# Optimization experiments

Measured on AMD Instinct MI355X. Metric: run time of the kernel, lower is better.

The kernel has to match this reference:

```python
import jax, jax.numpy as jnp
import numpy as np

B, N, OBS = 512, 64, 256
H1, H2 = 4, 4
D = 128            # embed/key dim (d_k_1 = d_k_2 = 128)
O1 = D // H1       # 32, per-head value dim stage 1
O2 = D // H2       # 32, per-head value dim stage 2
IN2 = O1 * H1      # 128, input dim to stage 2
FOUT = 16          # final_output_dim


def setup_inputs() -> dict:
    key = jax.random.key(0)
    ks = jax.random.split(key, 22)
    g = lambda k, shp: (jax.random.normal(k, shp, dtype=jnp.float32) * 0.05)
    inp = {
        "states": jax.random.normal(ks[0], (B, N, OBS), dtype=jnp.float32),
        # stage 1 per-head params, stacked over heads
        "E1_w": g(ks[1], (H1, D, OBS)), "E1_b": g(ks[2], (H1, D)),
        "K1_w": g(ks[3], (H1, D, D)),   "K1_b": g(ks[4], (H1, D)),
        "Q1_w": g(ks[5], (H1, D, D)),   "Q1_b": g(ks[6], (H1, D)),
        "V1_w": g(ks[7], (H1, O1, D)),  "V1_b": g(ks[8], (H1, O1)),
        # stage 2 per-head params
        "E2_w": g(ks[9], (H2, D, IN2)), "E2_b": g(ks[10], (H2, D)),
        "K2_w": g(ks[11], (H2, D, D)),  "K2_b": g(ks[12], (H2, D)),
        "Q2_w": g(ks[13], (H2, D, D)),  "Q2_b": g(ks[14], (H2, D)),
        "V2_w": g(ks[15], (H2, O2, D)), "V2_b": g(ks[16], (H2, O2)),
        # final MLP policy head
        "F1_w": g(ks[17], (64, O2 * H2)), "F1_b": g(ks[18], (64,)),
        "F2_w": g(ks[19], (FOUT, 64)),    "F2_b": g(ks[20], (FOUT,)),
    }
    return inp


def _attn_block(x, Ew, Eb, Kw, Kb, Qw, Qb, Vw, Vb, d_k):
    # x: [B,N,I]; all head loops batched via leading head axis h
    se = jax.nn.leaky_relu(jnp.einsum('bni,hdi->hbnd', x, Ew) + Eb[:, None, None, :])  # [h,B,N,D]
    k = jnp.einsum('hbnd,hed->hbne', se, Kw) + Kb[:, None, None, :]
    q = jnp.einsum('hbnd,hed->hbne', se, Qw) + Qb[:, None, None, :]
    w = jax.nn.softmax(jnp.einsum('hbne,hbme->hbnm', q, k) / jnp.sqrt(jnp.float32(d_k)), axis=-1)  # [h,B,N,N]
    v = jax.nn.leaky_relu(jnp.einsum('hbnd,hod->hbno', se, Vw) + Vb[:, None, None, :])  # [h,B,N,O]
    att = jnp.einsum('hbnm,hbmo->hbno', w, v)
    h, b, n, o = att.shape
    return jnp.transpose(att, (1, 2, 0, 3)).reshape(b, n, h * o), w


def reference(states, E1_w, E1_b, K1_w, K1_b, Q1_w, Q1_b, V1_w, V1_b,
              E2_w, E2_b, K2_w, K2_b, Q2_w, Q2_b, V2_w, V2_b,
              F1_w, F1_b, F2_w, F2_b):
    x1, w1 = _attn_block(states, E1_w, E1_b, K1_w, K1_b, Q1_w, Q1_b, V1_w, V1_b, D)
    x2, w2 = _attn_block(x1, E2_w, E2_b, K2_w, K2_b, Q2_w, Q2_b, V2_w, V2_b, D)
    h = jax.nn.leaky_relu(jnp.einsum('bnf,of->bno', x2, F1_w) + F1_b)
    policy = jax.nn.softmax(jnp.einsum('bno,po->bnp', h, F2_w) + F2_b, axis=-1)
    return policy, w1, w2
```

## Files before the change

kernel.cpp:

```cpp
#include <hip/hip_runtime.h>

typedef __attribute__((ext_vector_type(8))) short short8;
typedef __attribute__((ext_vector_type(4))) short short4v;
typedef __attribute__((ext_vector_type(4))) float f32x4;

#define MFMA(a, b, c) __builtin_amdgcn_mfma_f32_16x16x32_bf16((a), (b), (c), 0, 0, 0)

__device__ __forceinline__ short f2bf(float f) {
    union { float f; unsigned u; } v; v.f = f;
    unsigned r = v.u + 0x7fffu + ((v.u >> 16) & 1u);
    return (short)(r >> 16);
}
__device__ __forceinline__ float bf2f(short s) {
    union { unsigned u; float f; } v; v.u = ((unsigned)(unsigned short)s) << 16; return v.f;
}

struct ConvArgs { const float* src[10]; int end[10]; };

__global__ __launch_bounds__(256) void convert_weights_kernel(ConvArgs a, short* __restrict__ dst) {
    int i4 = blockIdx.x * 256 + threadIdx.x;
    int seg = 0;
#pragma unroll
    for (int s = 0; s < 9; s++) seg += (i4 >= a.end[s]) ? 1 : 0;
    int base = (seg == 0) ? 0 : a.end[seg - 1];
    float4 v = ((const float4*)a.src[seg])[i4 - base];
    short4v o; o.x = f2bf(v.x); o.y = f2bf(v.y); o.z = f2bf(v.z); o.w = f2bf(v.w);
    *(short4v*)(dst + (size_t)i4 * 4) = o;
}

#define KQ_LD  136
#define VT_LD  72
#define W_LD   72
#define OFF_K  0
#define OFF_Q  8704
#define OFF_SE 17408
#define OFF_VT 26112
#define OFF_W  8704
#define SMEM_SHORTS 28416

template<int IN, bool XF32>
__global__ __launch_bounds__(256) void attn_stage_kernel(
    const void* __restrict__ xin,
    const short* __restrict__ Ew, const float* __restrict__ Eb,
    const short* __restrict__ Kw, const float* __restrict__ Kb,
    const short* __restrict__ Qw, const float* __restrict__ Qb,
    const short* __restrict__ Vw, const float* __restrict__ Vb,
    float* __restrict__ w_out,
    short* __restrict__ x_out)
{
    __shared__ short sm[SMEM_SHORTS];
    const int tid  = threadIdx.x;
    const int b    = blockIdx.x >> 2;
    const int h    = blockIdx.x & 3;
    const int wv   = tid >> 6;
    const int lane = tid & 63;
    const int quad = lane >> 4;
    const int l16  = lane & 15;
    const int XLD  = IN + 8;

    if constexpr (XF32) {
        const float* xb = (const float*)xin + (size_t)b * 64 * IN;
#pragma unroll
        for (int r = 0; r < IN / 16; r++) {
            int f4 = tid + 256 * r;
            int row = f4 / (IN / 4), c4 = f4 % (IN / 4);
            float4 v = ((const float4*)xb)[f4];
            short4v o; o.x = f2bf(v.x); o.y = f2bf(v.y); o.z = f2bf(v.z); o.w = f2bf(v.w);
            *(short4v*)&sm[row * XLD + c4 * 4] = o;
        }
    } else {
        const short* xb = (const short*)xin + (size_t)b * 64 * IN;
#pragma unroll
        for (int r = 0; r < IN / 32; r++) {
            int f8 = tid + 256 * r;
            int row = f8 / (IN / 8), c8 = f8 % (IN / 8);
            short8 v = *(const short8*)(xb + (size_t)f8 * 8);
            *(short8*)&sm[row * XLD + c8 * 8] = v;
        }
    }
    __syncthreads();

    {
        const short* ewh = Ew + (size_t)h * 128 * IN;
        f32x4 acc[4][2];
#pragma unroll
        for (int j = 0; j < 2; j++) {
            float bv = Eb[h * 128 + wv * 32 + j * 16 + l16];
            f32x4 c = {bv, bv, bv, bv};
#pragma unroll
            for (int i = 0; i < 4; i++) acc[i][j] = c;
        }
        for (int k0 = 0; k0 < IN; k0 += 32) {
            short8 a[4], bb[2];
#pragma unroll
            for (int i = 0; i < 4; i++)
                a[i] = *(const short8*)&sm[(i * 16 + l16) * XLD + k0 + quad * 8];
#pragma unroll
            for (int j = 0; j < 2; j++)
                bb[j] = *(const short8*)(ewh + (size_t)(wv * 32 + j * 16 + l16) * IN + k0 + quad * 8);
#pragma unroll
            for (int i = 0; i < 4; i++)
#pragma unroll
                for (int j = 0; j < 2; j++)
                    acc[i][j] = MFMA(a[i], bb[j], acc[i][j]);
        }
#pragma unroll
        for (int i = 0; i < 4; i++)
#pragma unroll
            for (int j = 0; j < 2; j++)
#pragma unroll
                for (int r = 0; r < 4; r++) {
                    float v = acc[i][j][r];
                    v = (v >= 0.f) ? v : 0.01f * v;
                    sm[OFF_SE + (i * 16 + quad * 4 + r) * KQ_LD + wv * 32 + j * 16 + l16] = f2bf(v);
                }
    }
    __syncthreads();

    {
        const short* kwh = Kw + (size_t)h * 128 * 128;
        const short* qwh = Qw + (size_t)h * 128 * 128;
        f32x4 kacc[4][2], qacc[4][2];
#pragma unroll
        for (int j = 0; j < 2; j++) {
            float kb = Kb[h * 128 + wv * 32 + j * 16 + l16];
            float qb = Qb[h * 128 + wv * 32 + j * 16 + l16];
            f32x4 kc = {kb, kb, kb, kb}, qc = {qb, qb, qb, qb};
#pragma unroll
            for (int i = 0; i < 4; i++) { kacc[i][j] = kc; qacc[i][j] = qc; }
        }
#pragma unroll
        for (int k0 = 0; k0 < 128; k0 += 32) {
            short8 a[4], kb8[2], qb8[2];
#pragma unroll
            for (int i = 0; i < 4; i++)
                a[i] = *(const short8*)&sm[OFF_SE + (i * 16 + l16) * KQ_LD + k0 + quad * 8];
#pragma unroll
            for (int j = 0; j < 2; j++) {
                kb8[j] = *(const short8*)(kwh + (size_t)(wv * 32 + j * 16 + l16) * 128 + k0 + quad * 8);
                qb8[j] = *(const short8*)(qwh + (size_t)(wv * 32 + j * 16 + l16) * 128 + k0 + quad * 8);
            }
#pragma unroll
            for (int i = 0; i < 4; i++)
#pragma unroll
                for (int j = 0; j < 2; j++) {
                    kacc[i][j] = MFMA(a[i], kb8[j], kacc[i][j]);
                    qacc[i][j] = MFMA(a[i], qb8[j], qacc[i][j]);
                }
        }
#pragma unroll
        for (int i = 0; i < 4; i++)
#pragma unroll
            for (int j = 0; j < 2; j++)
#pragma unroll
                for (int r = 0; r < 4; r++) {
                    int row = i * 16 + quad * 4 + r, col = wv * 32 + j * 16 + l16;
                    sm[OFF_K + row * KQ_LD + col] = f2bf(kacc[i][j][r]);
                    sm[OFF_Q + row * KQ_LD + col] = f2bf(qacc[i][j][r]);
                }
        const short* vwh = Vw + (size_t)h * 32 * 128;
        const int n0v = (wv >> 1) * 16, mrow = (wv & 1) * 32;
        float vb = Vb[h * 32 + n0v + l16];
        f32x4 vacc[2]; vacc[0] = (f32x4){vb, vb, vb, vb}; vacc[1] = vacc[0];
#pragma unroll
        for (int k0 = 0; k0 < 128; k0 += 32) {
            short8 a0 = *(const short8*)&sm[OFF_SE + (mrow + l16) * KQ_LD + k0 + quad * 8];
            short8 a1 = *(const short8*)&sm[OFF_SE + (mrow + 16 + l16) * KQ_LD + k0 + quad * 8];
            short8 b8 = *(const short8*)(vwh + (size_t)(n0v + l16) * 128 + k0 + quad * 8);
            vacc[0] = MFMA(a0, b8, vacc[0]);
            vacc[1] = MFMA(a1, b8, vacc[1]);
        }
#pragma unroll
        for (int i = 0; i < 2; i++)
#pragma unroll
            for (int r = 0; r < 4; r++) {
                float v = vacc[i][r];
                v = (v >= 0.f) ? v : 0.01f * v;
                sm[OFF_VT + (n0v + l16) * VT_LD + mrow + i * 16 + quad * 4 + r] = f2bf(v);
            }
    }
    __syncthreads();

    f32x4 lacc[4];
#pragma unroll
    for (int jj = 0; jj < 4; jj++) lacc[jj] = (f32x4){0.f, 0.f, 0.f, 0.f};
#pragma unroll
    for (int k0 = 0; k0 < 128; k0 += 32) {
        short8 a = *(const short8*)&sm[OFF_Q + (wv * 16 + l16) * KQ_LD + k0 + quad * 8];
#pragma unroll
        for (int jj = 0; jj < 4; jj++) {
            short8 b8 = *(const short8*)&sm[OFF_K + (jj * 16 + l16) * KQ_LD + k0 + quad * 8];
            lacc[jj] = MFMA(a, b8, lacc[jj]);
        }
    }
    __syncthreads();

    {
        const float scale = 0.08838834764831845f;
        float mx[4], inv[4];
#pragma unroll
        for (int r = 0; r < 4; r++) {
            float m = lacc[0][r];
#pragma unroll
            for (int jj = 1; jj < 4; jj++) m = fmaxf(m, lacc[jj][r]);
#pragma unroll
            for (int s = 1; s < 16; s <<= 1) m = fmaxf(m, __shfl_xor(m, s, 16));
            mx[r] = m;
        }
        float sum[4] = {0.f, 0.f, 0.f, 0.f};
#pragma unroll
        for (int jj = 0; jj < 4; jj++)
#pragma unroll
            for (int r = 0; r < 4; r++) {
                float e = __expf((lacc[jj][r] - mx[r]) * scale);
                lacc[jj][r] = e; sum[r] += e;
            }
#pragma unroll
        for (int r = 0; r < 4; r++) {
#pragma unroll
            for (int s = 1; s < 16; s <<= 1) sum[r] += __shfl_xor(sum[r], s, 16);
            inv[r] = 1.0f / sum[r];
        }
        float* wbase = w_out + ((size_t)(h * 512 + b)) * 64 * 64;
#pragma unroll
        for (int r = 0; r < 4; r++) {
            int row = wv * 16 + quad * 4 + r;
#pragma unroll
            for (int jj = 0; jj < 4; jj++) {
                float wval = lacc[jj][r] * inv[r];
                wbase[(size_t)row * 64 + jj * 16 + l16] = wval;
                sm[OFF_W + row * W_LD + jj * 16 + l16] = f2bf(wval);
            }
        }
    }
    __syncthreads();

    {
        f32x4 aacc[2]; aacc[0] = (f32x4){0.f, 0.f, 0.f, 0.f}; aacc[1] = aacc[0];
#pragma unroll
        for (int k0 = 0; k0 < 64; k0 += 32) {
            short8 a = *(const short8*)&sm[OFF_W + (wv * 16 + l16) * W_LD + k0 + quad * 8];
#pragma unroll
            for (int j = 0; j < 2; j++) {
                short8 b8 = *(const short8*)&sm[OFF_VT + (j * 16 + l16) * VT_LD + k0 + quad * 8];
                aacc[j] = MFMA(a, b8, aacc[j]);
            }
        }
        short* xob = x_out + (size_t)b * 64 * 128;
#pragma unroll
        for (int j = 0; j < 2; j++)
#pragma unroll
            for (int r = 0; r < 4; r++)
                xob[(size_t)(wv * 16 + quad * 4 + r) * 128 + h * 32 + j * 16 + l16] = f2bf(aacc[j][r]);
    }
}

#define H_LD 72
__global__ __launch_bounds__(256)
void final_mlp_mfma_kernel(const short* __restrict__ x2,
                           const short* __restrict__ F1wb,
                           const float* __restrict__ F1b,
                           const short* __restrict__ F2wb,
                           const float* __restrict__ F2b,
                           float* __restrict__ policy)
{
    __shared__ short hsm[4][16 * H_LD];
    const int tid  = threadIdx.x;
    const int wv   = tid >> 6;
    const int lane = tid & 63;
    const int quad = lane >> 4;
    const int l16  = lane & 15;
    const int rowbase = blockIdx.x * 64 + wv * 16;

    short8 a[4];
    const short* xrow = x2 + (size_t)(rowbase + l16) * 128;
#pragma unroll
    for (int k = 0; k < 4; k++) a[k] = *(const short8*)(xrow + k * 32 + quad * 8);
    f32x4 acc[4];
#pragma unroll
    for (int j = 0; j < 4; j++) { float bv = F1b[j * 16 + l16]; acc[j] = (f32x4){bv, bv, bv, bv}; }
#pragma unroll
    for (int k = 0; k < 4; k++)
#pragma unroll
        for (int j = 0; j < 4; j++) {
            short8 b8 = *(const short8*)(F1wb + (size_t)(j * 16 + l16) * 128 + k * 32 + quad * 8);
            acc[j] = MFMA(a[k], b8, acc[j]);
        }
    short* hh = &hsm[wv][0];
#pragma unroll
    for (int j = 0; j < 4; j++)
#pragma unroll
        for (int r = 0; r < 4; r++) {
            float v = acc[j][r];
            v = (v >= 0.f) ? v : 0.01f * v;
            hh[(quad * 4 + r) * H_LD + j * 16 + l16] = f2bf(v);
        }
    __syncthreads();

    f32x4 lg;
    { float bv = F2b[l16]; lg = (f32x4){bv, bv, bv, bv}; }
#pragma unroll
    for (int k = 0; k < 2; k++) {
        short8 a2 = *(const short8*)(hh + l16 * H_LD + k * 32 + quad * 8);
        short8 b8 = *(const short8*)(F2wb + (size_t)l16 * 64 + k * 32 + quad * 8);
        lg = MFMA(a2, b8, lg);
    }
#pragma unroll
    for (int r = 0; r < 4; r++) {
        float m = lg[r];
        m = fmaxf(m, __shfl_xor(m, 1, 16));
        m = fmaxf(m, __shfl_xor(m, 2, 16));
        m = fmaxf(m, __shfl_xor(m, 4, 16));
        m = fmaxf(m, __shfl_xor(m, 8, 16));
        float e = __expf(lg[r] - m);
        float s = e;
        s += __shfl_xor(s, 1, 16);
        s += __shfl_xor(s, 2, 16);
        s += __shfl_xor(s, 4, 16);
        s += __shfl_xor(s, 8, 16);
        policy[(size_t)(rowbase + quad * 4 + r) * 16 + l16] = e / s;
    }
}

extern "C" void kernel_launch(void* const* d_in, const int* in_sizes, int n_in,
                              void* d_out, int out_size, void* d_ws, size_t ws_size,
                              hipStream_t stream) {
    const float* states = (const float*)d_in[0];
    const float* E1w = (const float*)d_in[1];  const float* E1b = (const float*)d_in[2];
    const float* K1w = (const float*)d_in[3];  const float* K1b = (const float*)d_in[4];
    const float* Q1w = (const float*)d_in[5];  const float* Q1b = (const float*)d_in[6];
    const float* V1w = (const float*)d_in[7];  const float* V1b = (const float*)d_in[8];
    const float* E2w = (const float*)d_in[9];  const float* E2b = (const float*)d_in[10];
    const float* K2w = (const float*)d_in[11]; const float* K2b = (const float*)d_in[12];
    const float* Q2w = (const float*)d_in[13]; const float* Q2b = (const float*)d_in[14];
    const float* V2w = (const float*)d_in[15]; const float* V2b = (const float*)d_in[16];
    const float* F1w = (const float*)d_in[17]; const float* F1b = (const float*)d_in[18];
    const float* F2w = (const float*)d_in[19]; const float* F2b = (const float*)d_in[20];

    float* out    = (float*)d_out;
    float* policy = out;
    float* w1     = out + 512 * 64 * 16;
    float* w2     = w1 + 4 * 512 * 64 * 64;

    short* wsb = (short*)d_ws;
    short* x1b = wsb;
    short* x2b = wsb + 4194304;
    short* wts = wsb + 8388608;
    short* wE1 = wts;            short* wK1 = wts + 131072;
    short* wQ1 = wts + 196608;   short* wV1 = wts + 262144;
    short* wE2 = wts + 278528;   short* wK2 = wts + 344064;
    short* wQ2 = wts + 409600;   short* wV2 = wts + 475136;
    short* wF1 = wts + 491520;   short* wF2 = wts + 499712;

    ConvArgs ca;
    ca.src[0] = E1w; ca.src[1] = K1w; ca.src[2] = Q1w; ca.src[3] = V1w;
    ca.src[4] = E2w; ca.src[5] = K2w; ca.src[6] = Q2w; ca.src[7] = V2w;
    ca.src[8] = F1w; ca.src[9] = F2w;
    ca.end[0] = 32768;  ca.end[1] = 49152;  ca.end[2] = 65536;  ca.end[3] = 69632;
    ca.end[4] = 86016;  ca.end[5] = 102400; ca.end[6] = 118784; ca.end[7] = 122880;
    ca.end[8] = 124928; ca.end[9] = 125184;
    convert_weights_kernel<<<489, 256, 0, stream>>>(ca, wts);

    attn_stage_kernel<256, true><<<2048, 256, 0, stream>>>(
        (const void*)states, wE1, E1b, wK1, K1b, wQ1, Q1b, wV1, V1b, w1, x1b);
    attn_stage_kernel<128, false><<<2048, 256, 0, stream>>>(
        (const void*)x1b, wE2, E2b, wK2, K2b, wQ2, Q2b, wV2, V2b, w2, x2b);
    final_mlp_mfma_kernel<<<512, 256, 0, stream>>>(x2b, wF1, F1b, wF2, F2b, policy);
}
```

Before: 232.6 us.

## Prefetch weight fragments into registers, alias V^T onto SE smem, raise occupancy

Weight fragments for the E, K, Q and V projections are loaded from global memory into registers up front, before the barrier or MFMA loop, so their latency overlaps other work instead of sitting inside each k-step. The V^T buffer now reuses the SE shared-memory region, with an extra barrier after the V projection, which cuts the LDS footprint. Launch bounds request 3 blocks per SM. The cost is much higher register pressure from the prefetched fragments, which may cause spills under the tighter occupancy bound.

```diff
diff --git a/kernel.cpp b/kernel.cpp
--- a/kernel.cpp
+++ b/kernel.cpp
@@ -34,12 +34,12 @@
 #define OFF_K  0
 #define OFF_Q  8704
 #define OFF_SE 17408
-#define OFF_VT 26112
+#define OFF_VT 17408
 #define OFF_W  8704
-#define SMEM_SHORTS 28416
+#define SMEM_SHORTS 26112
 
 template<int IN, bool XF32>
-__global__ __launch_bounds__(256) void attn_stage_kernel(
+__global__ __launch_bounds__(256, 3) void attn_stage_kernel(
     const void* __restrict__ xin,
     const short* __restrict__ Ew, const float* __restrict__ Eb,
     const short* __restrict__ Kw, const float* __restrict__ Kb,
@@ -57,6 +57,7 @@
     const int quad = lane >> 4;
     const int l16  = lane & 15;
     const int XLD  = IN + 8;
+    constexpr int NK1 = IN / 32;
 
     if constexpr (XF32) {
         const float* xb = (const float*)xin + (size_t)b * 64 * IN;
@@ -78,10 +79,19 @@
             *(short8*)&sm[row * XLD + c8 * 8] = v;
         }
     }
-    __syncthreads();
-
+
+    short8 ebf[NK1 * 2];
     {
         const short* ewh = Ew + (size_t)h * 128 * IN;
+#pragma unroll
+        for (int k0i = 0; k0i < NK1; k0i++)
+#pragma unroll
+            for (int j = 0; j < 2; j++)
+                ebf[k0i * 2 + j] = *(const short8*)(ewh + (size_t)(wv * 32 + j * 16 + l16) * IN + k0i * 32 + quad * 8);
+    }
+    __syncthreads();
+
+    {
         f32x4 acc[4][2];
 #pragma unroll
         for (int j = 0; j < 2; j++) {
@@ -90,19 +100,17 @@
 #pragma unroll
             for (int i = 0; i < 4; i++) acc[i][j] = c;
         }
-        for (int k0 = 0; k0 < IN; k0 += 32) {
-            short8 a[4], bb[2];
+#pragma unroll
+        for (int k0i = 0; k0i < NK1; k0i++) {
+            short8 a[4];
 #pragma unroll
             for (int i = 0; i < 4; i++)
-                a[i] = *(const short8*)&sm[(i * 16 + l16) * XLD + k0 + quad * 8];
-#pragma unroll
-            for (int j = 0; j < 2; j++)
-                bb[j] = *(const short8*)(ewh + (size_t)(wv * 32 + j * 16 + l16) * IN + k0 + quad * 8);
+                a[i] = *(const short8*)&sm[(i * 16 + l16) * XLD + k0i * 32 + quad * 8];
 #pragma unroll
             for (int i = 0; i < 4; i++)
 #pragma unroll
                 for (int j = 0; j < 2; j++)
-                    acc[i][j] = MFMA(a[i], bb[j], acc[i][j]);
+                    acc[i][j] = MFMA(a[i], ebf[k0i * 2 + j], acc[i][j]);
         }
 #pragma unroll
         for (int i = 0; i < 4; i++)
@@ -117,9 +125,18 @@
     }
     __syncthreads();
 
-    {
+    f32x4 vacc[2];
+    {
+        short8 kbf[8], qbf[8];
         const short* kwh = Kw + (size_t)h * 128 * 128;
         const short* qwh = Qw + (size_t)h * 128 * 128;
+#pragma unroll
+        for (int k0i = 0; k0i < 4; k0i++)
+#pragma unroll
+            for (int j = 0; j < 2; j++) {
+                kbf[k0i * 2 + j] = *(const short8*)(kwh + (size_t)(wv * 32 + j * 16 + l16) * 128 + k0i * 32 + quad * 8);
+                qbf[k0i * 2 + j] = *(const short8*)(qwh + (size_t)(wv * 32 + j * 16 + l16) * 128 + k0i * 32 + quad * 8);
+            }
         f32x4 kacc[4][2], qacc[4][2];
 #pragma unroll
         for (int j = 0; j < 2; j++) {
@@ -130,22 +147,17 @@
             for (int i = 0; i < 4; i++) { kacc[i][j] = kc; qacc[i][j] = qc; }
         }
 #pragma unroll
-        for (int k0 = 0; k0 < 128; k0 += 32) {
-            short8 a[4], kb8[2], qb8[2];
+        for (int k0i = 0; k0i < 4; k0i++) {
+            short8 a[4];
 #pragma unroll
             for (int i = 0; i < 4; i++)
-                a[i] = *(const short8*)&sm[OFF_SE + (i * 16 + l16) * KQ_LD + k0 + quad * 8];
-#pragma unroll
-            for (int j = 0; j < 2; j++) {
-                kb8[j] = *(const short8*)(kwh + (size_t)(wv * 32 + j * 16 + l16) * 128 + k0 + quad * 8);
-                qb8[j] = *(const short8*)(qwh + (size_t)(wv * 32 + j * 16 + l16) * 128 + k0 + quad * 8);
-            }
+                a[i] = *(const short8*)&sm[OFF_SE + (i * 16 + l16) * KQ_LD + k0i * 32 + quad * 8];
 #pragma unroll
             for (int i = 0; i < 4; i++)
 #pragma unroll
                 for (int j = 0; j < 2; j++) {
-                    kacc[i][j] = MFMA(a[i], kb8[j], kacc[i][j]);
-                    qacc[i][j] = MFMA(a[i], qb8[j], qacc[i][j]);
+                    kacc[i][j] = MFMA(a[i], kbf[k0i * 2 + j], kacc[i][j]);
+                    qacc[i][j] = MFMA(a[i], qbf[k0i * 2 + j], qacc[i][j]);
                 }
         }
 #pragma unroll
@@ -160,16 +172,24 @@
                 }
         const short* vwh = Vw + (size_t)h * 32 * 128;
         const int n0v = (wv >> 1) * 16, mrow = (wv & 1) * 32;
+        short8 vbf[4];
+#pragma unroll
+        for (int k0i = 0; k0i < 4; k0i++)
+            vbf[k0i] = *(const short8*)(vwh + (size_t)(n0v + l16) * 128 + k0i * 32 + quad * 8);
         float vb = Vb[h * 32 + n0v + l16];
-        f32x4 vacc[2]; vacc[0] = (f32x4){vb, vb, vb, vb}; vacc[1] = vacc[0];
-#pragma unroll
-        for (int k0 = 0; k0 < 128; k0 += 32) {
-            short8 a0 = *(const short8*)&sm[OFF_SE + (mrow + l16) * KQ_LD + k0 + quad * 8];
-            short8 a1 = *(const short8*)&sm[OFF_SE + (mrow + 16 + l16) * KQ_LD + k0 + quad * 8];
-            short8 b8 = *(const short8*)(vwh + (size_t)(n0v + l16) * 128 + k0 + quad * 8);
-            vacc[0] = MFMA(a0, b8, vacc[0]);
-            vacc[1] = MFMA(a1, b8, vacc[1]);
-        }
+        vacc[0] = (f32x4){vb, vb, vb, vb}; vacc[1] = vacc[0];
+#pragma unroll
+        for (int k0i = 0; k0i < 4; k0i++) {
+            short8 a0 = *(const short8*)&sm[OFF_SE + (mrow + l16) * KQ_LD + k0i * 32 + quad * 8];
+            short8 a1 = *(const short8*)&sm[OFF_SE + (mrow + 16 + l16) * KQ_LD + k0i * 32 + quad * 8];
+            vacc[0] = MFMA(a0, vbf[k0i], vacc[0]);
+            vacc[1] = MFMA(a1, vbf[k0i], vacc[1]);
+        }
+    }
+    __syncthreads();
+
+    {
+        const int n0v = (wv >> 1) * 16, mrow = (wv & 1) * 32;
 #pragma unroll
         for (int i = 0; i < 2; i++)
 #pragma unroll
@@ -179,7 +199,6 @@
                 sm[OFF_VT + (n0v + l16) * VT_LD + mrow + i * 16 + quad * 4 + r] = f2bf(v);
             }
     }
-    __syncthreads();
 
     f32x4 lacc[4];
 #pragma unroll
```

Measured after the change: 220.4 us. 1.06x faster.
